# Kernel tuning notes

Measured on AMD Instinct MI355X. Metric: run time of the kernel, lower is better.

The kernel has to match this reference:

```python
import jax, jax.numpy as jnp
import numpy as np

B, S, C = 8192, 7, 30


def _iou(b1, b2):
    """Faithful replica of calculate_iou (including its intersect/area1 + area2 - intersect quirk).
    b1, b2: [..., 4] as (cx, cy, w, h). Returns [...] ."""
    area1 = b1[..., 2] * b1[..., 3]
    area2 = b2[..., 2] * b2[..., 3]
    max_left = jnp.maximum(b1[..., 0] - b1[..., 2] / 2, b2[..., 0] - b2[..., 2] / 2)
    min_right = jnp.minimum(b1[..., 0] + b1[..., 2] / 2, b2[..., 0] + b2[..., 2] / 2)
    max_top = jnp.maximum(b1[..., 1] - b1[..., 3] / 2, b2[..., 1] - b2[..., 3] / 2)
    min_bottom = jnp.minimum(b1[..., 1] + b1[..., 3] / 2, b2[..., 1] + b2[..., 3] / 2)
    inter = (min_right - max_left) * (min_bottom - max_top)
    overlap = (max_left < min_right) & (max_top < min_bottom)
    return jnp.where(overlap, inter / area1 + area2 - inter, 0.0)


def setup_inputs() -> dict:
    key = jax.random.key(0)
    k1, k2, k3 = jax.random.split(key, 3)
    preds = jax.random.uniform(k1, (B, S, S, C), dtype=jnp.float32, minval=0.01, maxval=1.0)
    labels = jax.random.uniform(k2, (B, S, S, C), dtype=jnp.float32, minval=0.01, maxval=1.0)
    obj = (jax.random.uniform(k3, (B, S, S)) < 0.3).astype(jnp.float32)
    labels = labels.at[..., 4].set(obj)  # objectness indicator in {0,1}
    return {"preds": preds, "labels": labels}


def reference(preds, labels):
    batch_size = labels.shape[0]
    obj = (labels[..., 4] == 1).astype(preds.dtype)  # [B,7,7]

    # IoUs are computed on detached values in the original (numpy round-trip)
    iou1 = jax.lax.stop_gradient(_iou(preds[..., 0:4], labels[..., 0:4]))
    iou2 = jax.lax.stop_gradient(_iou(preds[..., 5:9], labels[..., 5:9]))
    resp1 = iou1 > iou2  # box 1 responsible

    xy1 = jnp.sum((preds[..., 0:2] - labels[..., 0:2]) ** 2, axis=-1)
    xy2 = jnp.sum((preds[..., 5:7] - labels[..., 5:7]) ** 2, axis=-1)
    wh1 = jnp.sum((jnp.sqrt(preds[..., 2:4]) - jnp.sqrt(labels[..., 2:4])) ** 2, axis=-1)
    wh2 = jnp.sum((jnp.sqrt(preds[..., 7:9]) - jnp.sqrt(labels[..., 7:9])) ** 2, axis=-1)

    loss_xy = 5.0 * jnp.where(resp1, xy1, xy2)
    loss_wh = jnp.where(resp1, wh1, wh2)
    loss_obj = jnp.where(resp1, (preds[..., 4] - iou1) ** 2, (preds[..., 9] - iou2) ** 2)
    loss_noobj_objcell = 0.5 * jnp.where(resp1, (preds[..., 9] - iou2) ** 2, (preds[..., 4] - iou1) ** 2)
    loss_cls = jnp.sum((preds[..., 10:] - labels[..., 10:]) ** 2, axis=-1)

    obj_cell = loss_xy + loss_wh + loss_obj + loss_noobj_objcell + loss_cls
    noobj_cell = 0.5 * (preds[..., 4] ** 2 + preds[..., 9] ** 2)

    total = jnp.sum(obj * obj_cell + (1.0 - obj) * noobj_cell)
    return total / batch_size
```

## Files before the change

kernel.cpp:

```cpp
#include <hip/hip_runtime.h>

#define YB      8192
#define YS      7
#define YC      30
#define NCELLS  (YB * YS * YS)
#define TCELLS  32
#define TBYTES  (TCELLS * YC * 4)
#define TFLOATS (TCELLS * YC)
#define NTILES  (NCELLS / TCELLS)
#define BLOCK   256
#define GRID    512
#define NWAVES  (GRID * 4)

__device__ __forceinline__ float iou_quirk(float cx1, float cy1, float w1, float h1,
                                           float cx2, float cy2, float w2, float h2) {
    float area1 = w1 * h1;
    float area2 = w2 * h2;
    float max_left   = fmaxf(cx1 - w1 * 0.5f, cx2 - w2 * 0.5f);
    float min_right  = fminf(cx1 + w1 * 0.5f, cx2 + w2 * 0.5f);
    float max_top    = fmaxf(cy1 - h1 * 0.5f, cy2 - h2 * 0.5f);
    float min_bottom = fminf(cy1 + h1 * 0.5f, cy2 + h2 * 0.5f);
    float inter = (min_right - max_left) * (min_bottom - max_top);
    bool overlap = (max_left < min_right) && (max_top < min_bottom);
    return overlap ? (inter / area1 + area2 - inter) : 0.0f;
}

__device__ __forceinline__ float cell_loss(const float* __restrict__ sp,
                                           const float* __restrict__ sl, int lane) {
    if (lane >= TCELLS) return 0.0f;
    const float2* p2 = (const float2*)(sp + lane * YC);
    const float2* l2 = (const float2*)(sl + lane * YC);

    float pv[10], lv[10];
    #pragma unroll
    for (int i = 0; i < 5; ++i) {
        float2 a = p2[i]; pv[2 * i] = a.x; pv[2 * i + 1] = a.y;
        float2 b = l2[i]; lv[2 * i] = b.x; lv[2 * i + 1] = b.y;
    }
    float loss_cls = 0.0f;
    #pragma unroll
    for (int i = 5; i < 15; ++i) {
        float2 a = p2[i], b = l2[i];
        float dx = a.x - b.x, dy = a.y - b.y;
        loss_cls += dx * dx + dy * dy;
    }

    float iou1 = iou_quirk(pv[0], pv[1], pv[2], pv[3], lv[0], lv[1], lv[2], lv[3]);
    float iou2 = iou_quirk(pv[5], pv[6], pv[7], pv[8], lv[5], lv[6], lv[7], lv[8]);
    bool resp1 = iou1 > iou2;

    float dx1 = pv[0] - lv[0], dy1 = pv[1] - lv[1];
    float xy1 = dx1 * dx1 + dy1 * dy1;
    float dx2 = pv[5] - lv[5], dy2 = pv[6] - lv[6];
    float xy2 = dx2 * dx2 + dy2 * dy2;

    float sw1 = sqrtf(pv[2]) - sqrtf(lv[2]), sh1 = sqrtf(pv[3]) - sqrtf(lv[3]);
    float wh1 = sw1 * sw1 + sh1 * sh1;
    float sw2 = sqrtf(pv[7]) - sqrtf(lv[7]), sh2 = sqrtf(pv[8]) - sqrtf(lv[8]);
    float wh2 = sw2 * sw2 + sh2 * sh2;

    float d1 = pv[4] - iou1, d2 = pv[9] - iou2;
    float e1 = d1 * d1, e2 = d2 * d2;

    float obj_cell = 5.0f * (resp1 ? xy1 : xy2)
                   + (resp1 ? wh1 : wh2)
                   + (resp1 ? e1 : e2)
                   + 0.5f * (resp1 ? e2 : e1)
                   + loss_cls;
    float noobj_cell = 0.5f * (pv[4] * pv[4] + pv[9] * pv[9]);

    return (lv[4] == 1.0f) ? obj_cell : noobj_cell;
}

__global__ __launch_bounds__(BLOCK) void yolo_partial_kernel(const float* __restrict__ preds,
                                                             const float* __restrict__ labels,
                                                             float* __restrict__ partial) {
    __shared__ float lds[4][2][2][TFLOATS];

    const int tid  = threadIdx.x;
    const int lane = tid & 63;
    const int w    = tid >> 6;
    const int wave_id = blockIdx.x * 4 + w;

    float acc = 0.0f;

#if defined(__has_builtin) && __has_builtin(__builtin_amdgcn_global_load_lds)
    typedef const __attribute__((address_space(1))) char* g_t;
    typedef __attribute__((address_space(3))) char* s_t;

    #define STAGE_ARR(gbase, sbase)                                                        \
        do {                                                                               \
            __builtin_amdgcn_global_load_lds((g_t)((gbase) + lane * 16),                   \
                                             (s_t)((sbase) + lane * 16), 16, 0, 0);        \
            __builtin_amdgcn_global_load_lds((g_t)((gbase) + 1024 + lane * 16),            \
                                             (s_t)((sbase) + 1024 + lane * 16), 16, 0, 0); \
            __builtin_amdgcn_global_load_lds((g_t)((gbase) + 2048 + lane * 16),            \
                                             (s_t)((sbase) + 2048 + lane * 16), 16, 0, 0); \
            __builtin_amdgcn_global_load_lds((g_t)((gbase) + 3072 + lane * 4),             \
                                             (s_t)((sbase) + 3072 + lane * 4), 4, 0, 0);   \
            __builtin_amdgcn_global_load_lds((g_t)((gbase) + 3328 + lane * 4),             \
                                             (s_t)((sbase) + 3328 + lane * 4), 4, 0, 0);   \
            __builtin_amdgcn_global_load_lds((g_t)((gbase) + 3584 + lane * 4),             \
                                             (s_t)((sbase) + 3584 + lane * 4), 4, 0, 0);   \
        } while (0)

    #define STAGE_TILE(tile, b)                                                            \
        do {                                                                               \
            const char* gp_ = (const char*)preds  + (size_t)(tile) * TBYTES;               \
            const char* gl_ = (const char*)labels + (size_t)(tile) * TBYTES;               \
            STAGE_ARR(gp_, (char*)&lds[w][(b)][0][0]);                                     \
            STAGE_ARR(gl_, (char*)&lds[w][(b)][1][0]);                                     \
        } while (0)

    int t = wave_id;
    int buf = 0;
    STAGE_TILE(t, 0);

    for (;;) {
        const int tn = t + NWAVES;
        if (tn >= NTILES) break;
        STAGE_TILE(tn, buf ^ 1);
        asm volatile("s_waitcnt vmcnt(12)" ::: "memory");
        __builtin_amdgcn_sched_barrier(0);
        acc += cell_loss(&lds[w][buf][0][0], &lds[w][buf][1][0], lane);
        buf ^= 1;
        t = tn;
    }
    asm volatile("s_waitcnt vmcnt(0)" ::: "memory");
    __builtin_amdgcn_sched_barrier(0);
    acc += cell_loss(&lds[w][buf][0][0], &lds[w][buf][1][0], lane);

    #undef STAGE_TILE
    #undef STAGE_ARR
#else
    for (int t = wave_id, buf = 0; t < NTILES; t += NWAVES, buf ^= 1) {
        const float4* gp = (const float4*)((const char*)preds  + (size_t)t * TBYTES);
        const float4* gl = (const float4*)((const char*)labels + (size_t)t * TBYTES);
        float4* sp4 = (float4*)&lds[w][buf][0][0];
        float4* sl4 = (float4*)&lds[w][buf][1][0];
        for (int i = lane; i < TFLOATS / 4; i += 64) { sp4[i] = gp[i]; sl4[i] = gl[i]; }
        asm volatile("s_waitcnt vmcnt(0) lgkmcnt(0)" ::: "memory");
        __builtin_amdgcn_sched_barrier(0);
        acc += cell_loss(&lds[w][buf][0][0], &lds[w][buf][1][0], lane);
    }
#endif

    for (int off = 32; off > 0; off >>= 1) acc += __shfl_down(acc, off);
    if (lane == 0) partial[wave_id] = acc;
}

__global__ __launch_bounds__(BLOCK) void yolo_final_kernel(const float* __restrict__ partial,
                                                           float* __restrict__ out) {
    __shared__ double w[BLOCK / 64];
    double s = 0.0;
    for (int i = threadIdx.x; i < NWAVES; i += BLOCK) s += (double)partial[i];
    for (int off = 32; off > 0; off >>= 1) s += __shfl_down(s, off);
    const int lane = threadIdx.x & 63, wid = threadIdx.x >> 6;
    if (lane == 0) w[wid] = s;
    __syncthreads();
    if (threadIdx.x == 0) out[0] = (float)((w[0] + w[1] + w[2] + w[3]) / (double)YB);
}

extern "C" void kernel_launch(void* const* d_in, const int* in_sizes, int n_in,
                              void* d_out, int out_size, void* d_ws, size_t ws_size,
                              hipStream_t stream) {
    const float* preds  = (const float*)d_in[0];
    const float* labels = (const float*)d_in[1];
    float* out = (float*)d_out;
    float* partial = (float*)d_ws;

    yolo_partial_kernel<<<GRID, BLOCK, 0, stream>>>(preds, labels, partial);
    yolo_final_kernel<<<1, BLOCK, 0, stream>>>(partial, out);
}
```

Before: 25.27 us.

## Replace global_load_lds double buffering with register prefetch and enlarge grid

Drops the direct global-to-LDS double buffer. Each wave now prefetches the next tile into registers with vector loads, writes the current tile into a single LDS buffer, and computes on it. This halves LDS per block, which may allow more resident blocks. The grid grows from 512 to 1280 blocks to put more memory requests in flight. The cost is extra VGPRs for the prefetched tile, an extra LDS write pass, and uneven work per wave, since each wave now handles only two or three tiles.

```diff
diff --git a/kernel.cpp b/kernel.cpp
--- a/kernel.cpp
+++ b/kernel.cpp
@@ -9,7 +9,7 @@
 #define TFLOATS (TCELLS * YC)
 #define NTILES  (NCELLS / TCELLS)
 #define BLOCK   256
-#define GRID    512
+#define GRID    1280
 #define NWAVES  (GRID * 4)
 
 __device__ __forceinline__ float iou_quirk(float cx1, float cy1, float w1, float h1,
@@ -75,78 +75,68 @@
 __global__ __launch_bounds__(BLOCK) void yolo_partial_kernel(const float* __restrict__ preds,
                                                              const float* __restrict__ labels,
                                                              float* __restrict__ partial) {
-    __shared__ float lds[4][2][2][TFLOATS];
+    __shared__ float lds[4][2][TFLOATS];
 
     const int tid  = threadIdx.x;
     const int lane = tid & 63;
     const int w    = tid >> 6;
-    const int wave_id = blockIdx.x * 4 + w;
+    const int gw   = blockIdx.x * 4 + w;
+
+    float* sp = &lds[w][0][0];
+    float* sl = &lds[w][1][0];
+
+    float4 rp0, rp1, rp2; float2 rp3; float rp4;
+    float4 rl0, rl1, rl2; float2 rl3; float rl4;
+
+    #define LOAD_TILE(t)                                                      \
+        do {                                                                  \
+            const char* gp_ = (const char*)preds  + (size_t)(t) * TBYTES;     \
+            const char* gl_ = (const char*)labels + (size_t)(t) * TBYTES;     \
+            rp0 = *(const float4*)(gp_ +    0 + lane * 16);                   \
+            rp1 = *(const float4*)(gp_ + 1024 + lane * 16);                   \
+            rp2 = *(const float4*)(gp_ + 2048 + lane * 16);                   \
+            rp3 = *(const float2*)(gp_ + 3072 + lane *  8);                   \
+            rp4 = *(const float*) (gp_ + 3584 + lane *  4);                   \
+            rl0 = *(const float4*)(gl_ +    0 + lane * 16);                   \
+            rl1 = *(const float4*)(gl_ + 1024 + lane * 16);                   \
+            rl2 = *(const float4*)(gl_ + 2048 + lane * 16);                   \
+            rl3 = *(const float2*)(gl_ + 3072 + lane *  8);                   \
+            rl4 = *(const float*) (gl_ + 3584 + lane *  4);                   \
+        } while (0)
+
+    #define WRITE_TILE()                                                      \
+        do {                                                                  \
+            *(float4*)((char*)sp +    0 + lane * 16) = rp0;                   \
+            *(float4*)((char*)sp + 1024 + lane * 16) = rp1;                   \
+            *(float4*)((char*)sp + 2048 + lane * 16) = rp2;                   \
+            *(float2*)((char*)sp + 3072 + lane *  8) = rp3;                   \
+            *(float*) ((char*)sp + 3584 + lane *  4) = rp4;                   \
+            *(float4*)((char*)sl +    0 + lane * 16) = rl0;                   \
+            *(float4*)((char*)sl + 1024 + lane * 16) = rl1;                   \
+            *(float4*)((char*)sl + 2048 + lane * 16) = rl2;                   \
+            *(float2*)((char*)sl + 3072 + lane *  8) = rl3;                   \
+            *(float*) ((char*)sl + 3584 + lane *  4) = rl4;                   \
+        } while (0)
 
     float acc = 0.0f;
 
-#if defined(__has_builtin) && __has_builtin(__builtin_amdgcn_global_load_lds)
-    typedef const __attribute__((address_space(1))) char* g_t;
-    typedef __attribute__((address_space(3))) char* s_t;
-
-    #define STAGE_ARR(gbase, sbase)                                                        \
-        do {                                                                               \
-            __builtin_amdgcn_global_load_lds((g_t)((gbase) + lane * 16),                   \
-                                             (s_t)((sbase) + lane * 16), 16, 0, 0);        \
-            __builtin_amdgcn_global_load_lds((g_t)((gbase) + 1024 + lane * 16),            \
-                                             (s_t)((sbase) + 1024 + lane * 16), 16, 0, 0); \
-            __builtin_amdgcn_global_load_lds((g_t)((gbase) + 2048 + lane * 16),            \
-                                             (s_t)((sbase) + 2048 + lane * 16), 16, 0, 0); \
-            __builtin_amdgcn_global_load_lds((g_t)((gbase) + 3072 + lane * 4),             \
-                                             (s_t)((sbase) + 3072 + lane * 4), 4, 0, 0);   \
-            __builtin_amdgcn_global_load_lds((g_t)((gbase) + 3328 + lane * 4),             \
-                                             (s_t)((sbase) + 3328 + lane * 4), 4, 0, 0);   \
-            __builtin_amdgcn_global_load_lds((g_t)((gbase) + 3584 + lane * 4),             \
-                                             (s_t)((sbase) + 3584 + lane * 4), 4, 0, 0);   \
-        } while (0)
-
-    #define STAGE_TILE(tile, b)                                                            \
-        do {                                                                               \
-            const char* gp_ = (const char*)preds  + (size_t)(tile) * TBYTES;               \
-            const char* gl_ = (const char*)labels + (size_t)(tile) * TBYTES;               \
-            STAGE_ARR(gp_, (char*)&lds[w][(b)][0][0]);                                     \
-            STAGE_ARR(gl_, (char*)&lds[w][(b)][1][0]);                                     \
-        } while (0)
-
-    int t = wave_id;
-    int buf = 0;
-    STAGE_TILE(t, 0);
-
+    int t = gw;
+    LOAD_TILE(t);
     for (;;) {
         const int tn = t + NWAVES;
+        WRITE_TILE();
+        if (tn < NTILES) LOAD_TILE(tn);
+        __builtin_amdgcn_sched_barrier(0);
+        acc += cell_loss(sp, sl, lane);
         if (tn >= NTILES) break;
-        STAGE_TILE(tn, buf ^ 1);
-        asm volatile("s_waitcnt vmcnt(12)" ::: "memory");
-        __builtin_amdgcn_sched_barrier(0);
-        acc += cell_loss(&lds[w][buf][0][0], &lds[w][buf][1][0], lane);
-        buf ^= 1;
         t = tn;
     }
-    asm volatile("s_waitcnt vmcnt(0)" ::: "memory");
-    __builtin_amdgcn_sched_barrier(0);
-    acc += cell_loss(&lds[w][buf][0][0], &lds[w][buf][1][0], lane);
 
-    #undef STAGE_TILE
-    #undef STAGE_ARR
-#else
-    for (int t = wave_id, buf = 0; t < NTILES; t += NWAVES, buf ^= 1) {
-        const float4* gp = (const float4*)((const char*)preds  + (size_t)t * TBYTES);
-        const float4* gl = (const float4*)((const char*)labels + (size_t)t * TBYTES);
-        float4* sp4 = (float4*)&lds[w][buf][0][0];
-        float4* sl4 = (float4*)&lds[w][buf][1][0];
-        for (int i = lane; i < TFLOATS / 4; i += 64) { sp4[i] = gp[i]; sl4[i] = gl[i]; }
-        asm volatile("s_waitcnt vmcnt(0) lgkmcnt(0)" ::: "memory");
-        __builtin_amdgcn_sched_barrier(0);
-        acc += cell_loss(&lds[w][buf][0][0], &lds[w][buf][1][0], lane);
-    }
-#endif
+    #undef LOAD_TILE
+    #undef WRITE_TILE
 
     for (int off = 32; off > 0; off >>= 1) acc += __shfl_down(acc, off);
-    if (lane == 0) partial[wave_id] = acc;
+    if (lane == 0) partial[gw] = acc;
 }
 
 __global__ __launch_bounds__(BLOCK) void yolo_final_kernel(const float* __restrict__ partial,
```

Measured after the change: 27.20 us. +7.6%, slower.
